# Kernel optimization log

Measured on AMD Instinct MI355X. Metric: run time of the kernel, lower is better.

## Reference

```python
import jax, jax.numpy as jnp
import numpy as np

ALPHA = 0.1  # LeakyReLU negative slope
F_OUT = 128

def _leaky(x):
    return jnp.where(x >= 0, x, ALPHA * x)

def setup_inputs() -> dict:
    key = jax.random.key(0)
    ks = jax.random.split(key, 12)
    B, N, F_IN = 4, 4096, 128
    q = jax.random.normal(ks[0], (B, N, F_IN), jnp.float32)
    k = jax.random.normal(ks[1], (B, N, F_IN), jnp.float32)
    v = jax.random.normal(ks[2], (B, N, F_IN), jnp.float32)
    adj = jax.random.randint(ks[3], (B, N, N), 0, 2, jnp.int32)
    s = 1.0 / np.sqrt(F_IN)
    Wq_w = jax.random.uniform(ks[4], (F_OUT, F_IN), jnp.float32, -s, s)
    Wq_b = jax.random.uniform(ks[5], (F_OUT,), jnp.float32, -s, s)
    Wk_w = jax.random.uniform(ks[6], (F_OUT, F_IN), jnp.float32, -s, s)
    Wk_b = jax.random.uniform(ks[7], (F_OUT,), jnp.float32, -s, s)
    Wv_w = jax.random.uniform(ks[8], (F_OUT, F_IN), jnp.float32, -s, s)
    Wv_b = jax.random.uniform(ks[9], (F_OUT,), jnp.float32, -s, s)
    # xavier_uniform with gain=1.414 on (2F,1)
    lim = 1.414 * np.sqrt(6.0 / (2 * F_OUT + 1))
    a = jax.random.uniform(ks[10], (2 * F_OUT, 1), jnp.float32, -lim, lim)
    so = 1.0 / np.sqrt(F_OUT)
    Wo_w = jax.random.uniform(ks[11], (F_OUT, F_OUT), jnp.float32, -so, so)
    return {"q": q, "k": k, "v": v, "adj": adj, "Wq_w": Wq_w, "Wq_b": Wq_b,
            "Wk_w": Wk_w, "Wk_b": Wk_b, "Wv_w": Wv_w, "Wv_b": Wv_b,
            "a": a, "Wo_w": Wo_w}

def reference(q, k, v, adj, Wq_w, Wq_b, Wk_w, Wk_b, Wv_w, Wv_b, a, Wo_w):
    qp = q @ Wq_w.T + Wq_b                      # (B,N,F)
    kp = k @ Wk_w.T + Wk_b
    vp = v @ Wv_w.T + Wv_b
    Wh1 = qp @ a[:F_OUT]                        # (B,N,1)
    Wh2 = kp @ a[F_OUT:]                        # (B,N,1)
    e = _leaky(Wh1 + jnp.swapaxes(Wh2, 1, 2))   # (B,N,N)
    e = jnp.where(adj > 0, e, jnp.float32(-1e9))
    att = jax.nn.softmax(e, axis=-1)
    h = jnp.einsum('bnm,bmf->bnf', att, vp)     # (B,N,F)
    return _leaky(h @ Wo_w.T)
```

## Files before the change

### kernel.cpp

```cpp
#include <hip/hip_runtime.h>


constexpr int B = 4, N = 4096, F = 128;
constexpr int BN = B * N;
constexpr int BK = 64;
constexpr int SPLITS = 8;
constexpr int JC = N / SPLITS;
constexpr int NIT = JC / BK;
#define ALPHA 0.1f

using float4v = __attribute__((ext_vector_type(4))) float;
using short8 = __attribute__((ext_vector_type(8))) short;
typedef unsigned long long ull;

__device__ __forceinline__ float leaky(float x) { return x >= 0.f ? x : ALPHA * x; }
__device__ __forceinline__ unsigned short f2bf(float x) {
    unsigned u = __float_as_uint(x);
    u = (u + 0x7FFFu + ((u >> 16) & 1u)) >> 16;
    return (unsigned short)u;
}
__device__ __forceinline__ unsigned pack_bf2(float lo, float hi) {
    unsigned a = __float_as_uint(lo), b2 = __float_as_uint(hi);
    a = a + 0x7FFFu + ((a >> 16) & 1u);
    b2 = b2 + 0x7FFFu + ((b2 >> 16) & 1u);
    return __builtin_amdgcn_perm(b2, a, 0x07060302u);
}

__global__ __launch_bounds__(256) void k_pack(const int* __restrict__ adj,
                                              ull* __restrict__ pack) {
    const long long GROUPS = (long long)B * N * N / 256;
    int t = threadIdx.x;
    int lane = t & 63;
    long long gw = ((long long)blockIdx.x * 256 + t) >> 6;
    long long nw = ((long long)gridDim.x * 256) >> 6;
    for (long long g = gw; g < GROUPS; g += nw) {
        long long base = g * 256;
        ull m0 = __ballot(adj[base + lane] != 0);
        ull m1 = __ballot(adj[base + 64 + lane] != 0);
        ull m2 = __ballot(adj[base + 128 + lane] != 0);
        ull m3 = __ballot(adj[base + 192 + lane] != 0);
        if (lane < 4) {
            ull w = (lane == 0) ? m0 : (lane == 1) ? m1 : (lane == 2) ? m2 : m3;
            pack[g * 4 + lane] = w;
        }
    }
}

__global__ __launch_bounds__(256) void k_ptrans(const ull* __restrict__ pack,
                                                ull* __restrict__ packT) {
    __shared__ ull tile[64][65];
    int t = threadIdx.x;
    int blk = blockIdx.x;
    int b = blk >> 6;
    int i0 = (blk & 63) * 64;
#pragma unroll
    for (int u = 0; u < 16; u++) {
        int unit = u * 256 + t;
        tile[unit >> 6][unit & 63] =
            pack[((size_t)b * N + i0 + (unit >> 6)) * 64 + (unit & 63)];
    }
    __syncthreads();
#pragma unroll
    for (int u = 0; u < 16; u++) {
        int unit = u * 256 + t;
        packT[((size_t)b * 64 + (unit >> 6)) * N + i0 + (unit & 63)] =
            tile[unit & 63][unit >> 6];
    }
}

__global__ void k_prep(const float* __restrict__ Wq_w, const float* __restrict__ Wq_b,
                       const float* __restrict__ Wk_w, const float* __restrict__ Wk_b,
                       const float* __restrict__ a, float* __restrict__ c1,
                       float* __restrict__ c2, float* __restrict__ d12) {
    __shared__ float as[2 * F];
    __shared__ float red[2 * F];
    int t = threadIdx.x;
    as[t] = a[t];
    __syncthreads();
    int f = t & 127;
    const float* W = (t < F) ? Wq_w : Wk_w;
    const float* ao = (t < F) ? as : as + F;
    float s = 0.f;
#pragma unroll 8
    for (int o = 0; o < F; o++) s = fmaf(W[o * F + f], ao[o], s);
    if (t < F) c1[f] = s; else c2[f] = s;
    red[t] = (t < F) ? Wq_b[f] * as[f] : Wk_b[f] * as[F + f];
    __syncthreads();
    for (int st = 64; st > 0; st >>= 1) {
        if (f < st) red[t] += red[t + st];
        __syncthreads();
    }
    if (t == 0) d12[0] = red[0];
    if (t == F) d12[1] = red[F];
}

__global__ void k_wh(const float* __restrict__ q, const float* __restrict__ k,
                     const float* __restrict__ c1, const float* __restrict__ c2,
                     const float* __restrict__ d12,
                     float* __restrict__ Wh1, float* __restrict__ Wh2) {
    __shared__ float c1s[F], c2s[F];
    int t = threadIdx.x;
    if (t < F) c1s[t] = c1[t]; else c2s[t - F] = c2[t - F];
    __syncthreads();
    int row = blockIdx.x * 8 + (t >> 5);
    int lane = t & 31;
    float4 q4 = reinterpret_cast<const float4*>(q)[row * 32 + lane];
    float4 k4 = reinterpret_cast<const float4*>(k)[row * 32 + lane];
    float s1 = q4.x * c1s[lane * 4 + 0] + q4.y * c1s[lane * 4 + 1] +
               q4.z * c1s[lane * 4 + 2] + q4.w * c1s[lane * 4 + 3];
    float s2 = k4.x * c2s[lane * 4 + 0] + k4.y * c2s[lane * 4 + 1] +
               k4.z * c2s[lane * 4 + 2] + k4.w * c2s[lane * 4 + 3];
    for (int m = 16; m > 0; m >>= 1) { s1 += __shfl_xor(s1, m); s2 += __shfl_xor(s2, m); }
    if (lane == 0) { Wh1[row] = s1 + d12[0]; Wh2[row] = s2 + d12[1]; }
}

__global__ void k_max2(const float* __restrict__ Wh2, float* __restrict__ M2) {
    int b = blockIdx.x, t = threadIdx.x;
    float m = -1e30f;
    for (int i = t; i < N; i += 256) m = fmaxf(m, Wh2[b * N + i]);
    __shared__ float red[256];
    red[t] = m;
    __syncthreads();
    for (int s = 128; s > 0; s >>= 1) { if (t < s) red[t] = fmaxf(red[t], red[t + s]); __syncthreads(); }
    if (t == 0) M2[b] = red[0];
}

__global__ void k_tab(const float* __restrict__ Wh1, const float* __restrict__ Wh2,
                      const float* __restrict__ M2,
                      float* __restrict__ P1, float* __restrict__ Q1,
                      float* __restrict__ P2, float* __restrict__ Q2) {
    int i = blockIdx.x * 256 + threadIdx.x;
    int b = i >> 12;
    float w1 = Wh1[i], w2 = Wh2[i];
    float mi = leaky(w1 + M2[b]);
    P1[i] = __expf(w1 - mi);
    Q1[i] = __expf(ALPHA * w1 - mi);
    P2[i] = __expf(w2);
    Q2[i] = __expf(ALPHA * w2);
}

__global__ __launch_bounds__(256) void k_vp(const float* __restrict__ v,
                                            const float* __restrict__ Wv_w,
                                            const float* __restrict__ Wv_b,
                                            unsigned short* __restrict__ vpT) {
    __shared__ float vs[32][F];
    __shared__ float Ws[F][129];
    __shared__ unsigned short ts[F][40];
    int t = threadIdx.x;
    int row0g = blockIdx.x * 32;
    int b = row0g >> 12;
    int row0 = row0g & (N - 1);
    {
        const float4* src = reinterpret_cast<const float4*>(v + row0g * F);
        float4* dst = reinterpret_cast<float4*>(&vs[0][0]);
#pragma unroll
        for (int u = 0; u < 4; u++) dst[u * 256 + t] = src[u * 256 + t];
    }
    {
        const float4* src = reinterpret_cast<const float4*>(Wv_w);
#pragma unroll
        for (int u = 0; u < 16; u++) {
            int unit = u * 256 + t;
            int r = unit >> 5, s = unit & 31;
            float4 val = src[unit];
            Ws[r][s * 4 + 0] = val.x; Ws[r][s * 4 + 1] = val.y;
            Ws[r][s * 4 + 2] = val.z; Ws[r][s * 4 + 3] = val.w;
        }
    }
    int f = t & 127, g = t >> 7;
    float bias = Wv_b[f];
    __syncthreads();
    float acc[16];
#pragma unroll
    for (int r = 0; r < 16; r++) acc[r] = bias;
    for (int kk = 0; kk < F; kk++) {
        float wk = Ws[f][kk];
#pragma unroll
        for (int r = 0; r < 16; r++) acc[r] = fmaf(vs[g * 16 + r][kk], wk, acc[r]);
    }
#pragma unroll
    for (int r = 0; r < 16; r++) ts[f][g * 16 + r] = f2bf(acc[r]);
    __syncthreads();
    int fr = t >> 1, hseg = t & 1;
    uint4 d0 = *reinterpret_cast<uint4*>(&ts[fr][hseg * 16]);
    uint4 d1 = *reinterpret_cast<uint4*>(&ts[fr][hseg * 16 + 8]);
    unsigned short* dst = vpT + ((size_t)(b * F + fr) * N + row0 + hseg * 16);
    *reinterpret_cast<uint4*>(dst) = d0;
    *reinterpret_cast<uint4*>(dst + 8) = d1;
}

__global__ __launch_bounds__(256, 4) void k_attn(
    const unsigned short* __restrict__ vpT, const ull* __restrict__ packT,
    const float* __restrict__ Wh1, const float* __restrict__ P1, const float* __restrict__ Q1,
    const float* __restrict__ P2, const float* __restrict__ Q2, const float* __restrict__ Wh2,
    float* __restrict__ h_part, float* __restrict__ den_part) {
    __shared__ __align__(16) unsigned short bs[F][72];
    __shared__ __align__(16) float sP2[JC], sQ2[JC], sW2[JC];
    int t = threadIdx.x;
    int idx = blockIdx.x;
    int split = idx & 7;
    int tile = (idx >> 3) & 31;
    int b = idx >> 8;
    int i0 = tile * 128;
    int jb0 = split * JC;
    int widx = t >> 6, lane = t & 63, m = lane & 15, q = lane >> 4;

    if (t < 128) {
        reinterpret_cast<float4*>(sP2)[t] = reinterpret_cast<const float4*>(P2 + b * N + jb0)[t];
        reinterpret_cast<float4*>(sQ2)[t] = reinterpret_cast<const float4*>(Q2 + b * N + jb0)[t];
        reinterpret_cast<float4*>(sW2)[t] = reinterpret_cast<const float4*>(Wh2 + b * N + jb0)[t];
    }

    int gi0 = b * N + i0 + widx * 32 + m;
    int gi1 = gi0 + 16;
    float p1a = P1[gi0], q1a = Q1[gi0], t1a = -Wh1[gi0];
    float p1b = P1[gi1], q1b = Q1[gi1], t1b = -Wh1[gi1];

    const ull* pt = packT + ((size_t)b * 64 + (size_t)split * 8) * N + i0 + widx * 32 + m;
    const unsigned short* vb = vpT + (size_t)b * F * N + jb0;

    uint4 sreg[4];
    auto load_stage = [&](int it) {
#pragma unroll
        for (int u = 0; u < 4; u++) {
            int unit = u * 256 + t;
            int r = unit >> 3, s = unit & 7;
            sreg[u] = *reinterpret_cast<const uint4*>(vb + (size_t)r * N + it * BK + s * 8);
        }
    };
    auto write_stage = [&]() {
#pragma unroll
        for (int u = 0; u < 4; u++) {
            int unit = u * 256 + t;
            int r = unit >> 3, s = unit & 7;
            *reinterpret_cast<uint4*>(&bs[r][s * 8]) = sreg[u];
        }
    };

    float4v acc0[8], acc1[8];
#pragma unroll
    for (int nt = 0; nt < 8; nt++) {
        acc0[nt] = (float4v){0.f, 0.f, 0.f, 0.f};
        acc1[nt] = (float4v){0.f, 0.f, 0.f, 0.f};
    }
    float den0 = 0.f, den1 = 0.f;

    auto gen_af = [&](unsigned bt, const float4& x2a, const float4& x2b,
                      const float4& p2a, const float4& p2b, const float4& q2a,
                      const float4& q2b, float p1, float q1, float t1, float& dn) -> short8 {
        float w0 = (bt & 1u)   ? ((x2a.x >= t1) ? p1 * p2a.x : q1 * q2a.x) : 0.f;
        float w1 = (bt & 2u)   ? ((x2a.y >= t1) ? p1 * p2a.y : q1 * q2a.y) : 0.f;
        float w2 = (bt & 4u)   ? ((x2a.z >= t1) ? p1 * p2a.z : q1 * q2a.z) : 0.f;
        float w3 = (bt & 8u)   ? ((x2a.w >= t1) ? p1 * p2a.w : q1 * q2a.w) : 0.f;
        float w4 = (bt & 16u)  ? ((x2b.x >= t1) ? p1 * p2b.x : q1 * q2b.x) : 0.f;
        float w5 = (bt & 32u)  ? ((x2b.y >= t1) ? p1 * p2b.y : q1 * q2b.y) : 0.f;
        float w6 = (bt & 64u)  ? ((x2b.z >= t1) ? p1 * p2b.z : q1 * q2b.z) : 0.f;
        float w7 = (bt & 128u) ? ((x2b.w >= t1) ? p1 * p2b.w : q1 * q2b.w) : 0.f;
        dn += ((w0 + w1) + (w2 + w3)) + ((w4 + w5) + (w6 + w7));
        union { short8 s; uint4 u; } r;
        r.u.x = pack_bf2(w0, w1); r.u.y = pack_bf2(w2, w3);
        r.u.z = pack_bf2(w4, w5); r.u.w = pack_bf2(w6, w7);
        return r.s;
    };

    ull pw0 = pt[0], pw1 = pt[16];
    ull nx0, nx1;
    load_stage(0);
    write_stage();
    __syncthreads();

#pragma unroll 1
    for (int it = 0; it < NIT; it++) {
        if (it + 1 < NIT) {
            load_stage(it + 1);
            nx0 = pt[(size_t)(it + 1) * N];
            nx1 = pt[(size_t)(it + 1) * N + 16];
        }
#pragma unroll
        for (int kh = 0; kh < 2; kh++) {
            int jl = it * BK + kh * 32 + q * 8;
            float4 x2a = *reinterpret_cast<const float4*>(&sW2[jl]);
            float4 x2b = *reinterpret_cast<const float4*>(&sW2[jl + 4]);
            float4 p2a = *reinterpret_cast<const float4*>(&sP2[jl]);
            float4 p2b = *reinterpret_cast<const float4*>(&sP2[jl + 4]);
            float4 q2a = *reinterpret_cast<const float4*>(&sQ2[jl]);
            float4 q2b = *reinterpret_cast<const float4*>(&sQ2[jl + 4]);
            unsigned bt0 = ((unsigned)(pw0 >> (kh * 32)) >> (q * 8)) & 0xFFu;
            unsigned bt1 = ((unsigned)(pw1 >> (kh * 32)) >> (q * 8)) & 0xFFu;
            short8 af0 = gen_af(bt0, x2a, x2b, p2a, p2b, q2a, q2b, p1a, q1a, t1a, den0);
            short8 af1 = gen_af(bt1, x2a, x2b, p2a, p2b, q2a, q2b, p1b, q1b, t1b, den1);
#pragma unroll
            for (int nt = 0; nt < 8; nt++) {
                short8 bf = *reinterpret_cast<const short8*>(&bs[nt * 16 + m][kh * 32 + q * 8]);
                acc0[nt] = __builtin_amdgcn_mfma_f32_16x16x32_bf16(af0, bf, acc0[nt], 0, 0, 0);
                acc1[nt] = __builtin_amdgcn_mfma_f32_16x16x32_bf16(af1, bf, acc1[nt], 0, 0, 0);
            }
        }
        if (it + 1 < NIT) {
            __syncthreads();
            write_stage();
            __syncthreads();
            pw0 = nx0; pw1 = nx1;
        }
    }

    den0 += __shfl_xor(den0, 16); den0 += __shfl_xor(den0, 32);
    den1 += __shfl_xor(den1, 16); den1 += __shfl_xor(den1, 32);
    float* dp = den_part + (size_t)split * BN;
    if (q == 0) { dp[gi0] = den0; dp[gi1] = den1; }
    float* hp = h_part + (size_t)split * BN * F;
    int orow = b * N + i0 + widx * 32 + q * 4;
#pragma unroll
    for (int nt = 0; nt < 8; nt++)
#pragma unroll
        for (int r = 0; r < 4; r++) {
            hp[(size_t)(orow + r) * F + nt * 16 + m] = acc0[nt][r];
            hp[(size_t)(orow + 16 + r) * F + nt * 16 + m] = acc1[nt][r];
        }
}

__global__ __launch_bounds__(256) void k_out(const float* __restrict__ h_part,
                                             const float* __restrict__ den_part,
                                             const float* __restrict__ Wo_w,
                                             float* __restrict__ out) {
    __shared__ float hs[32][F];
    __shared__ float Ws[F][129];
    int t = threadIdx.x;
    int row0 = blockIdx.x * 32;
    {
        const float4* src = reinterpret_cast<const float4*>(Wo_w);
#pragma unroll
        for (int u = 0; u < 16; u++) {
            int unit = u * 256 + t;
            int r = unit >> 5, s = unit & 31;
            float4 val = src[unit];
            Ws[r][s * 4 + 0] = val.x; Ws[r][s * 4 + 1] = val.y;
            Ws[r][s * 4 + 2] = val.z; Ws[r][s * 4 + 3] = val.w;
        }
    }
#pragma unroll
    for (int u = 0; u < 4; u++) {
        int unit = u * 256 + t;
        int r = unit >> 5, s = unit & 31;
        size_t off = (size_t)(row0 + r) * F + s * 4;
        float4 hv = *reinterpret_cast<const float4*>(h_part + off);
        float dsum = den_part[row0 + r];
#pragma unroll
        for (int sp = 1; sp < SPLITS; sp++) {
            float4 hx = *reinterpret_cast<const float4*>(h_part + (size_t)sp * BN * F + off);
            hv.x += hx.x; hv.y += hx.y; hv.z += hx.z; hv.w += hx.w;
            dsum += den_part[sp * BN + row0 + r];
        }
        float inv = 1.f / dsum;
        hs[r][s * 4 + 0] = hv.x * inv;
        hs[r][s * 4 + 1] = hv.y * inv;
        hs[r][s * 4 + 2] = hv.z * inv;
        hs[r][s * 4 + 3] = hv.w * inv;
    }
    __syncthreads();
    int f = t & 127, g = t >> 7;
    float acc[16];
#pragma unroll
    for (int r = 0; r < 16; r++) acc[r] = 0.f;
    for (int kk = 0; kk < F; kk++) {
        float wk = Ws[f][kk];
#pragma unroll
        for (int r = 0; r < 16; r++) acc[r] = fmaf(hs[g * 16 + r][kk], wk, acc[r]);
    }
#pragma unroll
    for (int r = 0; r < 16; r++) out[(size_t)(row0 + g * 16 + r) * F + f] = leaky(acc[r]);
}

extern "C" void kernel_launch(void* const* d_in, const int* in_sizes, int n_in,
                              void* d_out, int out_size, void* d_ws, size_t ws_size,
                              hipStream_t stream) {
    const float* q    = (const float*)d_in[0];
    const float* k    = (const float*)d_in[1];
    const float* v    = (const float*)d_in[2];
    const int*   adj  = (const int*)d_in[3];
    const float* Wq_w = (const float*)d_in[4];
    const float* Wq_b = (const float*)d_in[5];
    const float* Wk_w = (const float*)d_in[6];
    const float* Wk_b = (const float*)d_in[7];
    const float* Wv_w = (const float*)d_in[8];
    const float* Wv_b = (const float*)d_in[9];
    const float* a    = (const float*)d_in[10];
    const float* Wo_w = (const float*)d_in[11];
    float* out = (float*)d_out;
    float* ws = (float*)d_ws;

    unsigned short* vpT = (unsigned short*)ws;
    float* h_part   = ws + BN * F / 2;
    float* den_part = h_part + (size_t)SPLITS * BN * F;
    float* Wh1 = den_part + SPLITS * BN;
    float* Wh2 = Wh1 + BN;
    float* P1  = Wh2 + BN;
    float* Q1  = P1 + BN;
    float* P2  = Q1 + BN;
    float* Q2  = P2 + BN;
    float* c1  = Q2 + BN;
    float* c2  = c1 + F;
    float* d12 = c2 + F;
    float* M2  = d12 + 2;
    size_t off = (size_t)((M2 + B) - ws);
    off = (off + 3) & ~(size_t)3;
    ull* pack  = (ull*)(ws + off);
    ull* packT = pack + (size_t)BN * (N / 64);

    k_pack<<<2048, 256, 0, stream>>>(adj, pack);
    k_ptrans<<<B * 64, 256, 0, stream>>>(pack, packT);
    k_prep<<<1, 256, 0, stream>>>(Wq_w, Wq_b, Wk_w, Wk_b, a, c1, c2, d12);
    k_wh<<<BN / 8, 256, 0, stream>>>(q, k, c1, c2, d12, Wh1, Wh2);
    k_max2<<<B, 256, 0, stream>>>(Wh2, M2);
    k_tab<<<BN / 256, 256, 0, stream>>>(Wh1, Wh2, M2, P1, Q1, P2, Q2);
    k_vp<<<BN / 32, 256, 0, stream>>>(v, Wv_w, Wv_b, vpT);
    k_attn<<<B * 32 * SPLITS, 256, 0, stream>>>(vpT, packT, Wh1, P1, Q1, P2, Q2, Wh2,
                                                h_part, den_part);
    k_out<<<BN / 32, 256, 0, stream>>>(h_part, den_part, Wo_w, out);
}
```

Before: 597.0 us.

## Keep whole V chunk resident in LDS and loop over four row tiles per block

Each attention block now loads its full 512-column slice of the transposed V (128x512 bf16) into LDS once, then processes four 128-row tiles against it, double-buffering the adjacency bits and per-row scalars in registers. This removes the per-64-column staging loop and its two barriers per iteration, and reuses the V slice across four row tiles instead of reloading it. In exchange the grid shrinks from 1024 to 256 blocks with about 140 KB of LDS each, so each CU holds only one block and latency hiding relies on a single block's waves.

Result: faster. 553.1 us (-7.3%).

```diff
diff --git a/kernel.cpp b/kernel.cpp
--- a/kernel.cpp
+++ b/kernel.cpp
@@ -3,10 +3,10 @@
 
 constexpr int B = 4, N = 4096, F = 128;
 constexpr int BN = B * N;
-constexpr int BK = 64;
 constexpr int SPLITS = 8;
 constexpr int JC = N / SPLITS;
-constexpr int NIT = JC / BK;
+constexpr int ICH = 512;
+constexpr int NII = 4;
 #define ALPHA 0.1f
 
 using float4v = __attribute__((ext_vector_type(4))) float;
@@ -189,61 +189,59 @@
     *reinterpret_cast<uint4*>(dst + 8) = d1;
 }
 
-__global__ __launch_bounds__(256, 4) void k_attn(
+__global__ __launch_bounds__(256, 1) void k_attn(
     const unsigned short* __restrict__ vpT, const ull* __restrict__ packT,
     const float* __restrict__ Wh1, const float* __restrict__ P1, const float* __restrict__ Q1,
     const float* __restrict__ P2, const float* __restrict__ Q2, const float* __restrict__ Wh2,
     float* __restrict__ h_part, float* __restrict__ den_part) {
-    __shared__ __align__(16) unsigned short bs[F][72];
+    __shared__ __align__(16) unsigned short bs[F][JC + 8];
     __shared__ __align__(16) float sP2[JC], sQ2[JC], sW2[JC];
     int t = threadIdx.x;
     int idx = blockIdx.x;
     int split = idx & 7;
-    int tile = (idx >> 3) & 31;
-    int b = idx >> 8;
-    int i0 = tile * 128;
+    int ich = (idx >> 3) & 7;
+    int b = idx >> 6;
+    int i0 = ich * ICH;
     int jb0 = split * JC;
     int widx = t >> 6, lane = t & 63, m = lane & 15, q = lane >> 4;
 
+    const unsigned short* vb = vpT + (size_t)b * F * N + jb0;
+#pragma unroll
+    for (int u = 0; u < 32; u++) {
+        int unit = u * 256 + t;
+        int r = unit >> 6, c = unit & 63;
+        *reinterpret_cast<uint4*>(&bs[r][c * 8]) =
+            *reinterpret_cast<const uint4*>(vb + (size_t)r * N + c * 8);
+    }
     if (t < 128) {
         reinterpret_cast<float4*>(sP2)[t] = reinterpret_cast<const float4*>(P2 + b * N + jb0)[t];
         reinterpret_cast<float4*>(sQ2)[t] = reinterpret_cast<const float4*>(Q2 + b * N + jb0)[t];
         reinterpret_cast<float4*>(sW2)[t] = reinterpret_cast<const float4*>(Wh2 + b * N + jb0)[t];
     }
 
-    int gi0 = b * N + i0 + widx * 32 + m;
-    int gi1 = gi0 + 16;
-    float p1a = P1[gi0], q1a = Q1[gi0], t1a = -Wh1[gi0];
-    float p1b = P1[gi1], q1b = Q1[gi1], t1b = -Wh1[gi1];
-
-    const ull* pt = packT + ((size_t)b * 64 + (size_t)split * 8) * N + i0 + widx * 32 + m;
-    const unsigned short* vb = vpT + (size_t)b * F * N + jb0;
-
-    uint4 sreg[4];
-    auto load_stage = [&](int it) {
-#pragma unroll
-        for (int u = 0; u < 4; u++) {
-            int unit = u * 256 + t;
-            int r = unit >> 3, s = unit & 7;
-            sreg[u] = *reinterpret_cast<const uint4*>(vb + (size_t)r * N + it * BK + s * 8);
+    const ull* ptb = packT + ((size_t)b * 64 + (size_t)split * 8) * N;
+    auto load_bits = [&](int ii, ull* bw) {
+        int row = i0 + ii * 128 + widx * 32 + m;
+#pragma unroll
+        for (int cp = 0; cp < 8; cp++) {
+            bw[cp * 2 + 0] = ptb[(size_t)cp * N + row];
+            bw[cp * 2 + 1] = ptb[(size_t)cp * N + row + 16];
         }
     };
-    auto write_stage = [&]() {
-#pragma unroll
-        for (int u = 0; u < 4; u++) {
-            int unit = u * 256 + t;
-            int r = unit >> 3, s = unit & 7;
-            *reinterpret_cast<uint4*>(&bs[r][s * 8]) = sreg[u];
-        }
+    auto load_scal = [&](int ii, float* sc) {
+        int g0 = b * N + i0 + ii * 128 + widx * 32 + m;
+        sc[0] = P1[g0]; sc[1] = Q1[g0]; sc[2] = -Wh1[g0];
+        sc[3] = P1[g0 + 16]; sc[4] = Q1[g0 + 16]; sc[5] = -Wh1[g0 + 16];
     };
 
-    float4v acc0[8], acc1[8];
-#pragma unroll
-    for (int nt = 0; nt < 8; nt++) {
-        acc0[nt] = (float4v){0.f, 0.f, 0.f, 0.f};
-        acc1[nt] = (float4v){0.f, 0.f, 0.f, 0.f};
-    }
-    float den0 = 0.f, den1 = 0.f;
+    ull bwA[16], bwB[16];
+    float scA[6], scB[6];
+    load_bits(0, bwA);
+    load_scal(0, scA);
+    __syncthreads();
+
+    float* dp = den_part + (size_t)split * BN;
+    float* hp = h_part + (size_t)split * BN * F;
 
     auto gen_af = [&](unsigned bt, const float4& x2a, const float4& x2b,
                       const float4& p2a, const float4& p2b, const float4& q2a,
@@ -263,60 +261,57 @@
         return r.s;
     };
 
-    ull pw0 = pt[0], pw1 = pt[16];
-    ull nx0, nx1;
-    load_stage(0);
-    write_stage();
-    __syncthreads();
-
-#pragma unroll 1
-    for (int it = 0; it < NIT; it++) {
-        if (it + 1 < NIT) {
-            load_stage(it + 1);
-            nx0 = pt[(size_t)(it + 1) * N];
-            nx1 = pt[(size_t)(it + 1) * N + 16];
-        }
-#pragma unroll
-        for (int kh = 0; kh < 2; kh++) {
-            int jl = it * BK + kh * 32 + q * 8;
+    auto body = [&](int ii, ull* bw, float* sc, ull* bwn, float* scn) {
+        if (ii + 1 < NII) {
+            load_bits(ii + 1, bwn);
+            load_scal(ii + 1, scn);
+        }
+        float4v acc0[8], acc1[8];
+#pragma unroll
+        for (int nt = 0; nt < 8; nt++) {
+            acc0[nt] = (float4v){0.f, 0.f, 0.f, 0.f};
+            acc1[nt] = (float4v){0.f, 0.f, 0.f, 0.f};
+        }
+        float den0 = 0.f, den1 = 0.f;
+#pragma unroll 4
+        for (int c = 0; c < 16; c++) {
+            int jl = c * 32 + q * 8;
             float4 x2a = *reinterpret_cast<const float4*>(&sW2[jl]);
             float4 x2b = *reinterpret_cast<const float4*>(&sW2[jl + 4]);
             float4 p2a = *reinterpret_cast<const float4*>(&sP2[jl]);
             float4 p2b = *reinterpret_cast<const float4*>(&sP2[jl + 4]);
             float4 q2a = *reinterpret_cast<const float4*>(&sQ2[jl]);
             float4 q2b = *reinterpret_cast<const float4*>(&sQ2[jl + 4]);
-            unsigned bt0 = ((unsigned)(pw0 >> (kh * 32)) >> (q * 8)) & 0xFFu;
-            unsigned bt1 = ((unsigned)(pw1 >> (kh * 32)) >> (q * 8)) & 0xFFu;
-            short8 af0 = gen_af(bt0, x2a, x2b, p2a, p2b, q2a, q2b, p1a, q1a, t1a, den0);
-            short8 af1 = gen_af(bt1, x2a, x2b, p2a, p2b, q2a, q2b, p1b, q1b, t1b, den1);
+            int cp = c >> 1, hf = c & 1;
+            unsigned bt0 = ((unsigned)(bw[cp * 2 + 0] >> (hf * 32)) >> (q * 8)) & 0xFFu;
+            unsigned bt1 = ((unsigned)(bw[cp * 2 + 1] >> (hf * 32)) >> (q * 8)) & 0xFFu;
+            short8 af0 = gen_af(bt0, x2a, x2b, p2a, p2b, q2a, q2b, sc[0], sc[1], sc[2], den0);
+            short8 af1 = gen_af(bt1, x2a, x2b, p2a, p2b, q2a, q2b, sc[3], sc[4], sc[5], den1);
 #pragma unroll
             for (int nt = 0; nt < 8; nt++) {
-                short8 bf = *reinterpret_cast<const short8*>(&bs[nt * 16 + m][kh * 32 + q * 8]);
+                short8 bf = *reinterpret_cast<const short8*>(&bs[nt * 16 + m][jl]);
                 acc0[nt] = __builtin_amdgcn_mfma_f32_16x16x32_bf16(af0, bf, acc0[nt], 0, 0, 0);
                 acc1[nt] = __builtin_amdgcn_mfma_f32_16x16x32_bf16(af1, bf, acc1[nt], 0, 0, 0);
             }
         }
-        if (it + 1 < NIT) {
-            __syncthreads();
-            write_stage();
-            __syncthreads();
-            pw0 = nx0; pw1 = nx1;
-        }
-    }
-
-    den0 += __shfl_xor(den0, 16); den0 += __shfl_xor(den0, 32);
-    den1 += __shfl_xor(den1, 16); den1 += __shfl_xor(den1, 32);
-    float* dp = den_part + (size_t)split * BN;
-    if (q == 0) { dp[gi0] = den0; dp[gi1] = den1; }
-    float* hp = h_part + (size_t)split * BN * F;
-    int orow = b * N + i0 + widx * 32 + q * 4;
-#pragma unroll
-    for (int nt = 0; nt < 8; nt++)
-#pragma unroll
-        for (int r = 0; r < 4; r++) {
-            hp[(size_t)(orow + r) * F + nt * 16 + m] = acc0[nt][r];
-            hp[(size_t)(orow + 16 + r) * F + nt * 16 + m] = acc1[nt][r];
-        }
+        den0 += __shfl_xor(den0, 16); den0 += __shfl_xor(den0, 32);
+        den1 += __shfl_xor(den1, 16); den1 += __shfl_xor(den1, 32);
+        int g0 = b * N + i0 + ii * 128 + widx * 32 + m;
+        if (q == 0) { dp[g0] = den0; dp[g0 + 16] = den1; }
+        int orow = b * N + i0 + ii * 128 + widx * 32 + q * 4;
+#pragma unroll
+        for (int nt = 0; nt < 8; nt++)
+#pragma unroll
+            for (int r = 0; r < 4; r++) {
+                hp[(size_t)(orow + r) * F + nt * 16 + m] = acc0[nt][r];
+                hp[(size_t)(orow + 16 + r) * F + nt * 16 + m] = acc1[nt][r];
+            }
+    };
+
+    body(0, bwA, scA, bwB, scB);
+    body(1, bwB, scB, bwA, scA);
+    body(2, bwA, scA, bwB, scB);
+    body(3, bwB, scB, bwA, scA);
 }
 
 __global__ __launch_bounds__(256) void k_out(const float* __restrict__ h_part,
@@ -414,7 +409,7 @@
     k_max2<<<B, 256, 0, stream>>>(Wh2, M2);
     k_tab<<<BN / 256, 256, 0, stream>>>(Wh1, Wh2, M2, P1, Q1, P2, Q2);
     k_vp<<<BN / 32, 256, 0, stream>>>(v, Wv_w, Wv_b, vpT);
-    k_attn<<<B * 32 * SPLITS, 256, 0, stream>>>(vpT, packT, Wh1, P1, Q1, P2, Q2, Wh2,
-                                                h_part, den_part);
+    k_attn<<<B * 8 * SPLITS, 256, 0, stream>>>(vpT, packT, Wh1, P1, Q1, P2, Q2, Wh2,
+                                               h_part, den_part);
     k_out<<<BN / 32, 256, 0, stream>>>(h_part, den_part, Wo_w, out);
 }
```
